# Performance work log

Hardware: AMD Instinct MI355X
Metric: run time of the kernel (lower is better)

Reference implementation:

```python
import jax, jax.numpy as jnp
import numpy as np
from jax import lax

DILATIONS = [1, 2, 4]
L, H, D_IN = 3, 256, 256
T, B = 512, 128


def _lstm_scan(gx, whh, bhh, h0, c0):
    """gx: (Td, N, 4H) precomputed input gates; scan torch LSTMCell recurrence."""
    def step(carry, g_x):
        h, c = carry
        gates = g_x + h @ whh.T + bhh          # (N, 4H), gate order i,f,g,o
        i, f, g, o = jnp.split(gates, 4, axis=-1)
        c = jax.nn.sigmoid(f) * c + jax.nn.sigmoid(i) * jnp.tanh(g)
        h = jax.nn.sigmoid(o) * jnp.tanh(c)
        return (h, c), h
    (_, _), hs = lax.scan(step, (h0, c0), gx)
    return hs                                   # (Td, N, H)


def _dilated_layer(x, wih, whh, b_ih, b_hh, rate):
    """x: (T, B, D). Pack `rate` consecutive steps along batch, run cell, unpack."""
    t, b, d = x.shape
    td = -(-t // rate)                          # ceil division
    pad = td * rate - t
    if pad:
        x = jnp.pad(x, ((0, pad), (0, 0), (0, 0)))
    h = wih.shape[0] // 4
    # torch.cat([x[i*r+j] for j in range(r)], dim=0) == reshape (td, r*b, d)
    xd = x.reshape(td, rate * b, d)
    gx = xd @ wih.T + b_ih                      # hoist input projection out of scan
    h0 = jnp.zeros((rate * b, h), x.dtype)
    hs = _lstm_scan(gx, whh, b_hh, h0, jnp.zeros_like(h0))
    # torch.chunk(out, r, 0) unroll == reshape back to (td*r, b, h), trim pad
    return hs.reshape(td * rate, b, h)[:t]


def setup_inputs() -> dict:
    key = jax.random.key(0)
    ks = jax.random.split(key, 5)
    s = 1.0 / np.sqrt(H)                        # torch LSTMCell init scale
    return {
        "x":   jax.random.normal(ks[0], (T, B, D_IN), jnp.float32),
        "Wih": jax.random.uniform(ks[1], (L, 4 * H, D_IN), jnp.float32, -s, s),
        "Whh": jax.random.uniform(ks[2], (L, 4 * H, H), jnp.float32, -s, s),
        "bih": jax.random.uniform(ks[3], (L, 4 * H), jnp.float32, -s, s),
        "bhh": jax.random.uniform(ks[4], (L, 4 * H), jnp.float32, -s, s),
    }


def reference(x, Wih, Whh, bih, bhh):
    outs = []
    cur = x
    for l, rate in enumerate(DILATIONS):
        cur = _dilated_layer(cur, Wih[l], Whh[l], bih[l], bhh[l], rate)
        outs.append(cur)
    return jnp.stack(outs, axis=0)              # (L, T, B, H)
```

## Files before the change

kernel.cpp:

```cpp
#include <hip/hip_runtime.h>


typedef _Float16 half8   __attribute__((ext_vector_type(8)));
typedef _Float16 half4_t __attribute__((ext_vector_type(4)));
typedef float    floatx4 __attribute__((ext_vector_type(4)));

__device__ __forceinline__ float sigmf(float x) {
    return 1.0f / (1.0f + __expf(-x));
}
__device__ __forceinline__ float tanhfast(float x) {
    float e = __expf(-2.0f * fabsf(x));
    float r = (1.0f - e) / (1.0f + e);
    return copysignf(r, x);
}

#define MFMA16(A, B, C) __builtin_amdgcn_mfma_f32_16x16x32_f16((A), (B), (C), 0, 0, 0)

typedef __attribute__((address_space(3))) unsigned int lds_u32;
typedef __attribute__((address_space(1))) unsigned int glb_u32;

__device__ __forceinline__ void gload_lds16(const _Float16* g, _Float16* l) {
    __builtin_amdgcn_global_load_lds((const glb_u32*)g, (lds_u32*)l, 16, 0, 0);
}

#define RING_SLOTS 4
#define RING_STRIDE (512 * 256)
#define RING_BYTES  (RING_SLOTS * RING_STRIDE * 2)
#define CNT_PER_LAYER 8192
#define CNT_INTS      24576

__global__ void prep_kernel(
    const float* __restrict__ Wih, const float* __restrict__ Whh,
    const float* __restrict__ bih, const float* __restrict__ bhh,
    _Float16* __restrict__ wihp, _Float16* __restrict__ whhp,
    float* __restrict__ biasc)
{
    int id = blockIdx.x * 256 + threadIdx.x;
    if (id < 196608) {
        int u = id;
        const float* W = Whh; _Float16* P = whhp;
        if (u >= 98304) { W = Wih; P = wihp; u -= 98304; }
        int ln = u & 63; u >>= 6;
        int ks = u & 7;  u >>= 3;
        int ct = u & 7;  u >>= 3;
        int w  = u & 7;  u >>= 3;
        int l  = u;
        int col = (ct >> 1) * 256 + w * 32 + (ct & 1) * 16 + (ln & 15);
        int k0  = ks * 32 + (ln >> 4) * 8;
        const float* src = W + ((size_t)l * 1024 + col) * 256 + k0;
        half8 hv;
#pragma unroll
        for (int j = 0; j < 8; ++j) hv[j] = (_Float16)src[j];
        *(half8*)(P + (size_t)l * 262144 +
                  (size_t)(((w * 8 + ct) * 8 + ks) * 64 + ln) * 8) = hv;
    } else if (id < 199680) {
        int v = id - 196608;
        biasc[v] = bih[v] + bhh[v];
    }
}

template<int F16IN>
__global__ __attribute__((amdgpu_flat_work_group_size(512, 512)))
__attribute__((amdgpu_waves_per_eu(2, 2)))
void gx_kernel(
    const float* __restrict__ in32,
    const _Float16* __restrict__ in16,
    const _Float16* __restrict__ wpack,
    const float* __restrict__ biasc,
    _Float16* __restrict__ gx,
    int rate, int SG, int S)
{
    __shared__ _Float16 Ab[64][264];
    const int tid = threadIdx.x, lane = tid & 63, w = tid >> 6;
    const int t = blockIdx.x / SG, sg = blockIdx.x % SG;
    const int r15 = lane & 15, q = lane >> 4;

#pragma unroll
    for (int i = 0; i < 4; ++i) {
        int id = tid + 512 * i;
        int row = id >> 5, c16 = id & 31;
        int n = sg * 64 + row;
        size_t base = ((size_t)(t * rate + (n >> 7)) * 128 + (n & 127)) * 256 + c16 * 8;
        if (F16IN) {
            *(uint4*)&Ab[row][c16 * 8] = *(const uint4*)(in16 + base);
        } else {
            floatx4 v0 = *(const floatx4*)(in32 + base);
            floatx4 v1 = *(const floatx4*)(in32 + base + 4);
            half8 hv;
            hv[0] = (_Float16)v0[0]; hv[1] = (_Float16)v0[1];
            hv[2] = (_Float16)v0[2]; hv[3] = (_Float16)v0[3];
            hv[4] = (_Float16)v1[0]; hv[5] = (_Float16)v1[1];
            hv[6] = (_Float16)v1[2]; hv[7] = (_Float16)v1[3];
            *(half8*)&Ab[row][c16 * 8] = hv;
        }
    }
    __syncthreads();

    floatx4 zero4 = {0.f, 0.f, 0.f, 0.f};
    floatx4 acc[4][8];
#pragma unroll
    for (int rt = 0; rt < 4; ++rt)
#pragma unroll
        for (int ct = 0; ct < 8; ++ct) acc[rt][ct] = zero4;

    const _Float16* wsp = wpack + (size_t)w * 32768 + (size_t)lane * 8;
    half8 bfA[8], bfB[8];
#pragma unroll
    for (int ct = 0; ct < 8; ++ct)
        bfA[ct] = *(const half8*)(wsp + (ct * 8 + 0) * 512);

#define AKS(ks, bufC, bufN) { \
    if ((ks) + 1 < 8) { _Pragma("unroll") \
        for (int ct = 0; ct < 8; ++ct) \
            bufN[ct] = *(const half8*)(wsp + (ct * 8 + ((ks) + 1)) * 512); } \
    half8 a0 = *(const half8*)&Ab[ 0 + r15][(ks) * 32 + q * 8]; \
    half8 a1 = *(const half8*)&Ab[16 + r15][(ks) * 32 + q * 8]; \
    half8 a2 = *(const half8*)&Ab[32 + r15][(ks) * 32 + q * 8]; \
    half8 a3 = *(const half8*)&Ab[48 + r15][(ks) * 32 + q * 8]; \
    _Pragma("unroll") for (int ct = 0; ct < 8; ++ct) { \
        acc[0][ct] = MFMA16(a0, bufC[ct], acc[0][ct]); \
        acc[1][ct] = MFMA16(a1, bufC[ct], acc[1][ct]); \
        acc[2][ct] = MFMA16(a2, bufC[ct], acc[2][ct]); \
        acc[3][ct] = MFMA16(a3, bufC[ct], acc[3][ct]); } }

    AKS(0, bfA, bfB); AKS(1, bfB, bfA); AKS(2, bfA, bfB); AKS(3, bfB, bfA);
    AKS(4, bfA, bfB); AKS(5, bfB, bfA); AKS(6, bfA, bfB); AKS(7, bfB, bfA);
#undef AKS

    float be[4], bo_[4];
#pragma unroll
    for (int cp = 0; cp < 4; ++cp) {
        be[cp]  = biasc[cp * 256 + w * 32 + r15];
        bo_[cp] = biasc[cp * 256 + w * 32 + 16 + r15];
    }
#pragma unroll
    for (int rt = 0; rt < 4; ++rt) {
        int sb = sg * 4 + rt;
#pragma unroll
        for (int cp = 0; cp < 4; ++cp) {
            half8 hv;
#pragma unroll
            for (int rg = 0; rg < 4; ++rg) {
                hv[rg]     = (_Float16)(acc[rt][2 * cp][rg]     + be[cp]);
                hv[4 + rg] = (_Float16)(acc[rt][2 * cp + 1][rg] + bo_[cp]);
            }
            *(half8*)(gx + ((((size_t)t * S + sb) * 8 + w) * 4 + cp) * 512 +
                      (size_t)lane * 8) = hv;
        }
    }
}

__global__ __attribute__((amdgpu_flat_work_group_size(512, 512)))
__attribute__((amdgpu_waves_per_eu(2, 2)))
void scan2_kernel(
    const _Float16* __restrict__ gx,
    const _Float16* __restrict__ wpack,
    float* __restrict__ out,
    _Float16* __restrict__ h16,
    _Float16* __restrict__ ring,
    int* __restrict__ cnt,
    int rate, int td, int NB8)
{
    __shared__ _Float16 own[2][16][136];
    __shared__ _Float16 Gx[4][4][64][8];

    const int tid  = threadIdx.x;
    const int lane = tid & 63;
    const int w    = tid >> 6;
    const int r15  = lane & 15;
    const int q    = lane >> 4;
    const int bg   = blockIdx.x % NB8;
    const int hh   = blockIdx.x / NB8;
    const int n0   = bg * 16;
    const int myb  = blockIdx.x;
    const int sib  = (hh ^ 1) * NB8 + bg;
    const int hidg = hh * 128 + w * 16 + r15;

    half8 wf[4][8];
    {
        const int w8 = hh * 4 + (w >> 1), b = w & 1;
#pragma unroll
        for (int g = 0; g < 4; ++g)
#pragma unroll
            for (int ks = 0; ks < 8; ++ks)
                wf[g][ks] = *(const half8*)(wpack +
                    (size_t)(((w8 * 8 + 2 * g + b) * 8 + ks) * 64 + lane) * 8);
    }

    for (int i = tid; i < 16 * 136; i += 512)
        (&own[0][0][0])[i] = (_Float16)0.0f;

#pragma unroll
    for (int j = 0; j < 2; ++j) {
        int gi = w * 2 + j, a = gi >> 2, part = gi & 3;
        const _Float16* src = gx +
            ((((size_t)0 * NB8 + bg) * 8 + (hh * 4 + a)) * 4 + part) * 512 +
            (size_t)lane * 8;
        gload_lds16(src, &Gx[a][part][0][0]);
    }

    float cst[4] = {0.f, 0.f, 0.f, 0.f};
    float hv[4];

    for (int t = 0; t < td; ++t) {
        const int rd = t & 1, wr = rd ^ 1;

        half8 af[8];
        if (t > 0) {
            const int ci = sib * td + (t - 1);
            if (tid == 0) {
                while (__hip_atomic_load(&cnt[ci], __ATOMIC_RELAXED,
                                         __HIP_MEMORY_SCOPE_AGENT) < 1) {
                    __builtin_amdgcn_s_sleep(1);
                }
            }
            __syncthreads();
            (void)__hip_atomic_load(&cnt[ci], __ATOMIC_ACQUIRE,
                                    __HIP_MEMORY_SCOPE_AGENT);
            const _Float16* rs = ring + (size_t)((t - 1) & 3) * RING_STRIDE +
                                 (size_t)(n0 + r15) * 256;
            if (hh == 0) {
                af[4] = *(const half8*)(rs + 4 * 32 + q * 8);
                af[5] = *(const half8*)(rs + 5 * 32 + q * 8);
                af[6] = *(const half8*)(rs + 6 * 32 + q * 8);
                af[7] = *(const half8*)(rs + 7 * 32 + q * 8);
            } else {
                af[0] = *(const half8*)(rs + 0 * 32 + q * 8);
                af[1] = *(const half8*)(rs + 1 * 32 + q * 8);
                af[2] = *(const half8*)(rs + 2 * 32 + q * 8);
                af[3] = *(const half8*)(rs + 3 * 32 + q * 8);
            }
        } else {
            __syncthreads();
            half8 z;
#pragma unroll
            for (int j = 0; j < 8; ++j) z[j] = (_Float16)0.0f;
            if (hh == 0) { af[4] = z; af[5] = z; af[6] = z; af[7] = z; }
            else         { af[0] = z; af[1] = z; af[2] = z; af[3] = z; }
        }

        floatx4 acc[4];
#pragma unroll
        for (int g = 0; g < 4; ++g) {
            half4_t gv = *(const half4_t*)&Gx[w >> 1][g][lane][(w & 1) * 4];
#pragma unroll
            for (int rg = 0; rg < 4; ++rg) acc[g][rg] = (float)gv[rg];
        }

        if (hh == 0) {
            af[0] = *(const half8*)&own[rd][r15][0 * 32 + q * 8];
            af[1] = *(const half8*)&own[rd][r15][1 * 32 + q * 8];
            af[2] = *(const half8*)&own[rd][r15][2 * 32 + q * 8];
            af[3] = *(const half8*)&own[rd][r15][3 * 32 + q * 8];
        } else {
            af[4] = *(const half8*)&own[rd][r15][0 * 32 + q * 8];
            af[5] = *(const half8*)&own[rd][r15][1 * 32 + q * 8];
            af[6] = *(const half8*)&own[rd][r15][2 * 32 + q * 8];
            af[7] = *(const half8*)&own[rd][r15][3 * 32 + q * 8];
        }

#define DO_KS(ks) { \
        acc[0] = MFMA16(af[ks], wf[0][ks], acc[0]); \
        acc[1] = MFMA16(af[ks], wf[1][ks], acc[1]); \
        acc[2] = MFMA16(af[ks], wf[2][ks], acc[2]); \
        acc[3] = MFMA16(af[ks], wf[3][ks], acc[3]); }
        if (hh == 0) {
            DO_KS(0) DO_KS(1) DO_KS(2) DO_KS(3)
            DO_KS(4) DO_KS(5) DO_KS(6) DO_KS(7)
        } else {
            DO_KS(4) DO_KS(5) DO_KS(6) DO_KS(7)
            DO_KS(0) DO_KS(1) DO_KS(2) DO_KS(3)
        }
#undef DO_KS

        _Float16* rngw = ring + (size_t)(t & 3) * RING_STRIDE;
#pragma unroll
        for (int rg = 0; rg < 4; ++rg) {
            float gi = acc[0][rg], gf = acc[1][rg];
            float gg = acc[2][rg], go = acc[3][rg];
            float c = sigmf(gf) * cst[rg] + sigmf(gi) * tanhfast(gg);
            cst[rg] = c;
            float h = sigmf(go) * tanhfast(c);
            hv[rg] = h;
            own[wr][q * 4 + rg][w * 16 + r15] = (_Float16)h;
            rngw[(size_t)(n0 + q * 4 + rg) * 256 + hidg] = (_Float16)h;
        }

        __syncthreads();
        if (tid == 0) {
            __hip_atomic_fetch_add(&cnt[myb * td + t], 1, __ATOMIC_RELEASE,
                                   __HIP_MEMORY_SCOPE_AGENT);
        }

#pragma unroll
        for (int rg = 0; rg < 4; ++rg) {
            int n = n0 + q * 4 + rg;
            int tau = t * rate + (n >> 7);
            size_t off = ((size_t)tau * 128 + (n & 127)) * 256 + hidg;
            out[off] = hv[rg];
            h16[off] = (_Float16)hv[rg];
        }

        if (t + 1 < td) {
#pragma unroll
            for (int j = 0; j < 2; ++j) {
                int gi = w * 2 + j, a = gi >> 2, part = gi & 3;
                const _Float16* src = gx +
                    ((((size_t)(t + 1) * NB8 + bg) * 8 + (hh * 4 + a)) * 4 + part) * 512 +
                    (size_t)lane * 8;
                gload_lds16(src, &Gx[a][part][0][0]);
            }
        }
    }
}

#define GH 16
#define NB 32
#define FB_CNT_INTS 6144

__global__ __launch_bounds__(256) void lstm_layer_kernel(
    const float* __restrict__ in,
    const float* __restrict__ Wih,
    const float* __restrict__ Whh,
    const float* __restrict__ bih,
    const float* __restrict__ bhh,
    float* __restrict__ out,
    _Float16* __restrict__ ring,
    int* __restrict__ cnt,
    int rate, int td, int G_b)
{
    __shared__ _Float16 Abuf[NB][520];
    __shared__ float scr[NB][68];

    const int tid  = threadIdx.x;
    const int lane = tid & 63;
    const int wv   = tid >> 6;
    const int g_b  = blockIdx.x % G_b;
    const int g_h  = blockIdx.x / G_b;
    const int hid0 = g_h * 16;
    const int n0   = g_b * NB;

    half8 bfrag[16];
    {
        const int col  = lane & 15;
        const int qq   = lane >> 4;
        const int grow = wv * 256 + hid0 + col;
        const float* wih_row = Wih + (size_t)grow * 256;
        const float* whh_row = Whh + (size_t)grow * 256;
#pragma unroll
        for (int ks = 0; ks < 16; ++ks) {
            const int k0 = ks * 32 + qq * 8;
            const float* src = (k0 < 256) ? (wih_row + k0) : (whh_row + (k0 - 256));
            floatx4 w0 = *(const floatx4*)(src);
            floatx4 w1 = *(const floatx4*)(src + 4);
            half8 hb;
            hb[0] = (_Float16)w0[0]; hb[1] = (_Float16)w0[1];
            hb[2] = (_Float16)w0[2]; hb[3] = (_Float16)w0[3];
            hb[4] = (_Float16)w1[0]; hb[5] = (_Float16)w1[1];
            hb[6] = (_Float16)w1[2]; hb[7] = (_Float16)w1[3];
            bfrag[ks] = hb;
        }
    }

    const int erow = tid >> 4;
    const int ehid = tid & 15;
    const float bi = bih[0 * 256 + hid0 + ehid] + bhh[0 * 256 + hid0 + ehid];
    const float bf = bih[1 * 256 + hid0 + ehid] + bhh[1 * 256 + hid0 + ehid];
    const float bg = bih[2 * 256 + hid0 + ehid] + bhh[2 * 256 + hid0 + ehid];
    const float bo = bih[3 * 256 + hid0 + ehid] + bhh[3 * 256 + hid0 + ehid];
    float c0 = 0.0f, c1 = 0.0f;

    floatx4 xp[8];
#pragma unroll
    for (int i = 0; i < 8; ++i) {
        int id  = tid + 256 * i;
        int row = id >> 6;
        int m   = n0 + row;
        const float* p = in + ((size_t)(0 * rate + (m >> 7)) * 128 + (m & 127)) * 256
                         + (size_t)(id & 63) * 4;
        xp[i] = *(const floatx4*)p;
    }

    for (int t = 0; t < td; ++t) {
#pragma unroll
        for (int i = 0; i < 8; ++i) {
            int id  = tid + 256 * i;
            int row = id >> 6;
            int c4  = (id & 63) * 4;
            half4_t hx;
            hx[0] = (_Float16)xp[i][0]; hx[1] = (_Float16)xp[i][1];
            hx[2] = (_Float16)xp[i][2]; hx[3] = (_Float16)xp[i][3];
            *(half4_t*)&Abuf[row][c4] = hx;
        }
        if (t + 1 < td) {
#pragma unroll
            for (int i = 0; i < 8; ++i) {
                int id  = tid + 256 * i;
                int row = id >> 6;
                int m   = n0 + row;
                const float* p = in + ((size_t)((t + 1) * rate + (m >> 7)) * 128 + (m & 127)) * 256
                                 + (size_t)(id & 63) * 4;
                xp[i] = *(const floatx4*)p;
            }
        }
        if (t > 0) {
            const int ci = g_b * td + (t - 1);
            if (tid == 0) {
                while (__hip_atomic_load(&cnt[ci], __ATOMIC_RELAXED,
                                         __HIP_MEMORY_SCOPE_AGENT) < GH) {
                    __builtin_amdgcn_s_sleep(1);
                }
            }
            __syncthreads();
            (void)__hip_atomic_load(&cnt[ci], __ATOMIC_ACQUIRE, __HIP_MEMORY_SCOPE_AGENT);
            const _Float16* rs = ring + (size_t)((t - 1) & 3) * RING_STRIDE;
#pragma unroll
            for (int i = 0; i < 4; ++i) {
                int id  = tid + 256 * i;
                int row = id >> 5;
                int kc  = id & 31;
                int m   = n0 + row;
                uint4 v = *(const uint4*)(rs + (size_t)m * 256 + kc * 8);
                *(uint4*)&Abuf[row][256 + kc * 8] = v;
            }
        } else {
#pragma unroll
            for (int i = 0; i < 4; ++i) {
                int id  = tid + 256 * i;
                int row = id >> 5;
                int kc  = id & 31;
                uint4 z = {0u, 0u, 0u, 0u};
                *(uint4*)&Abuf[row][256 + kc * 8] = z;
            }
        }
        __syncthreads();

        floatx4 acc0 = {0.f, 0.f, 0.f, 0.f};
        floatx4 acc1 = {0.f, 0.f, 0.f, 0.f};
        {
            const int r  = lane & 15;
            const int qq = lane >> 4;
#pragma unroll
            for (int ks = 0; ks < 16; ++ks) {
                half8 a0 = *(const half8*)&Abuf[r][ks * 32 + qq * 8];
                half8 a1 = *(const half8*)&Abuf[16 + r][ks * 32 + qq * 8];
                acc0 = MFMA16(a0, bfrag[ks], acc0);
                acc1 = MFMA16(a1, bfrag[ks], acc1);
            }
        }
        {
            const int r  = lane & 15;
            const int qq = lane >> 4;
#pragma unroll
            for (int reg = 0; reg < 4; ++reg) {
                scr[qq * 4 + reg][wv * 16 + r]      = acc0[reg];
                scr[16 + qq * 4 + reg][wv * 16 + r] = acc1[reg];
            }
        }
        __syncthreads();

        {
            float gi0 = scr[erow][ehid]           + bi;
            float gf0 = scr[erow][16 + ehid]      + bf;
            float gg0 = scr[erow][32 + ehid]      + bg;
            float go0 = scr[erow][48 + ehid]      + bo;
            float gi1 = scr[16 + erow][ehid]      + bi;
            float gf1 = scr[16 + erow][16 + ehid] + bf;
            float gg1 = scr[16 + erow][32 + ehid] + bg;
            float go1 = scr[16 + erow][48 + ehid] + bo;

            c0 = sigmf(gf0) * c0 + sigmf(gi0) * tanhfast(gg0);
            c1 = sigmf(gf1) * c1 + sigmf(gi1) * tanhfast(gg1);
            float h0v = sigmf(go0) * tanhfast(c0);
            float h1v = sigmf(go1) * tanhfast(c1);

            int m0 = n0 + erow, m1 = m0 + 16;
            int tau0 = t * rate + (m0 >> 7);
            int tau1 = t * rate + (m1 >> 7);
            out[((size_t)tau0 * 128 + (m0 & 127)) * 256 + hid0 + ehid] = h0v;
            out[((size_t)tau1 * 128 + (m1 & 127)) * 256 + hid0 + ehid] = h1v;

            _Float16* rw_ = ring + (size_t)(t & 3) * RING_STRIDE;
            rw_[(size_t)m0 * 256 + hid0 + ehid] = (_Float16)h0v;
            rw_[(size_t)m1 * 256 + hid0 + ehid] = (_Float16)h1v;
        }

        __syncthreads();
        if (tid == 0) {
            __hip_atomic_fetch_add(&cnt[g_b * td + t], 1, __ATOMIC_RELEASE,
                                   __HIP_MEMORY_SCOPE_AGENT);
        }
    }
}

extern "C" void kernel_launch(void* const* d_in, const int* in_sizes, int n_in,
                              void* d_out, int out_size, void* d_ws, size_t ws_size,
                              hipStream_t stream) {
    const float* x   = (const float*)d_in[0];
    const float* Wih = (const float*)d_in[1];
    const float* Whh = (const float*)d_in[2];
    const float* bih = (const float*)d_in[3];
    const float* bhh = (const float*)d_in[4];
    float* out = (float*)d_out;

    const size_t GX_BYTES   = 134217728ull;
    const size_t H16_BYTES  = 33554432ull;
    const size_t WP_BYTES   = 1572864ull;
    const size_t BIAS_BYTES = 12288ull;
    const size_t NEED = GX_BYTES + H16_BYTES + 2 * WP_BYTES + BIAS_BYTES +
                        RING_BYTES + CNT_INTS * sizeof(int);

    if (ws_size >= NEED) {
        char* p = (char*)d_ws;
        _Float16* gxb  = (_Float16*)p;                 p += GX_BYTES;
        _Float16* h16  = (_Float16*)p;                 p += H16_BYTES;
        _Float16* whhp = (_Float16*)p;                 p += WP_BYTES;
        _Float16* wihp = (_Float16*)p;                 p += WP_BYTES;
        float*    biasc= (float*)p;                    p += BIAS_BYTES;
        _Float16* ring = (_Float16*)p;                 p += RING_BYTES;
        int*      cnt  = (int*)p;

        hipMemsetAsync(cnt, 0, CNT_INTS * sizeof(int), stream);
        prep_kernel<<<dim3(780), dim3(256), 0, stream>>>(
            Wih, Whh, bih, bhh, wihp, whhp, biasc);

        const int rates[3] = {1, 2, 4};
        for (int l = 0; l < 3; ++l) {
            const int rate = rates[l];
            const int td   = 512 / rate;
            const int NB8  = rate * 8;
            const int SG   = NB8 / 4;
            float* out_l = out + (size_t)l * 512 * 128 * 256;
            if (l == 0)
                gx_kernel<0><<<dim3(td * SG), dim3(512), 0, stream>>>(
                    x, nullptr, wihp + (size_t)l * 262144, biasc + l * 1024,
                    gxb, rate, SG, NB8);
            else
                gx_kernel<1><<<dim3(td * SG), dim3(512), 0, stream>>>(
                    nullptr, h16, wihp + (size_t)l * 262144, biasc + l * 1024,
                    gxb, rate, SG, NB8);
            scan2_kernel<<<dim3(2 * NB8), dim3(512), 0, stream>>>(
                gxb, whhp + (size_t)l * 262144, out_l, h16, ring,
                cnt + l * CNT_PER_LAYER, rate, td, NB8);
        }
        return;
    }

    _Float16* ring = (_Float16*)d_ws;
    int* cnt = (int*)((char*)d_ws + RING_BYTES);
    hipMemsetAsync(cnt, 0, FB_CNT_INTS * sizeof(int), stream);

    const int rates[3]  = {1, 2, 4};
    const int cntOff[3] = {0, 2048, 4096};
    const float* in_ptr = x;
    for (int l = 0; l < 3; ++l) {
        const int rate = rates[l];
        const int td   = 512 / rate;
        const int N    = rate * 128;
        const int G_b  = N / NB;
        lstm_layer_kernel<<<dim3(G_b * GH), dim3(256), 0, stream>>>(
            in_ptr,
            Wih + (size_t)l * 1024 * 256,
            Whh + (size_t)l * 1024 * 256,
            bih + (size_t)l * 1024,
            bhh + (size_t)l * 1024,
            out + (size_t)l * 512 * 128 * 256,
            ring, cnt + cntOff[l],
            rate, td, G_b);
        in_ptr = out + (size_t)l * 512 * 128 * 256;
    }
}
```

Measured before the change: 5.221 ms.

## Split LSTM scan across four hidden-quarter blocks with swizzled LDS h exchange

The recurrent scan now splits each batch group's hidden dimension across four 256-thread blocks instead of two 512-thread blocks. Each block waits on its three peers per step, then stages the full previous h from a two-slot global ring into XOR-swizzled LDS via direct global-to-LDS loads. Gate activations are regrouped through an fp32 LDS scratch so each thread does vectorized elementwise math and vector stores. The input-projection kernel is retiled into four times as many blocks, each computing a narrower column slice. The intent is more CUs working on the latency-bound recurrence, at the cost of more cross-block synchronization, extra barriers and global-memory traffic for the h exchange.

```diff
diff --git a/kernel.cpp b/kernel.cpp
--- a/kernel.cpp
+++ b/kernel.cpp
@@ -23,11 +23,11 @@
     __builtin_amdgcn_global_load_lds((const glb_u32*)g, (lds_u32*)l, 16, 0, 0);
 }
 
-#define RING_SLOTS 4
 #define RING_STRIDE (512 * 256)
-#define RING_BYTES  (RING_SLOTS * RING_STRIDE * 2)
-#define CNT_PER_LAYER 8192
-#define CNT_INTS      24576
+#define BR_SLOTS    2
+#define BR_RING_BYTES (BR_SLOTS * RING_STRIDE * 2)
+#define CNT_PER_LAYER 16384
+#define CNT_INTS      49152
 
 __global__ void prep_kernel(
     const float* __restrict__ Wih, const float* __restrict__ Whh,
@@ -60,26 +60,28 @@
 }
 
 template<int F16IN>
-__global__ __attribute__((amdgpu_flat_work_group_size(512, 512)))
-__attribute__((amdgpu_waves_per_eu(2, 2)))
-void gx_kernel(
+__global__ __launch_bounds__(512, 1) void gx_kernel(
     const float* __restrict__ in32,
     const _Float16* __restrict__ in16,
     const _Float16* __restrict__ wpack,
     const float* __restrict__ biasc,
     _Float16* __restrict__ gx,
-    int rate, int SG, int S)
+    int rate, int RB, int NB8)
 {
     __shared__ _Float16 Ab[64][264];
     const int tid = threadIdx.x, lane = tid & 63, w = tid >> 6;
-    const int t = blockIdx.x / SG, sg = blockIdx.x % SG;
+    const int cb  = blockIdx.x & 3;
+    const int nbi = (blockIdx.x >> 2) % RB;
+    const int t   = (blockIdx.x >> 2) / RB;
     const int r15 = lane & 15, q = lane >> 4;
+    const int w8  = 2 * cb + (w & 1);
+    const int cp  = w >> 1;
 
 #pragma unroll
     for (int i = 0; i < 4; ++i) {
         int id = tid + 512 * i;
         int row = id >> 5, c16 = id & 31;
-        int n = sg * 64 + row;
+        int n = nbi * 64 + row;
         size_t base = ((size_t)(t * rate + (n >> 7)) * 128 + (n & 127)) * 256 + c16 * 8;
         if (F16IN) {
             *(uint4*)&Ab[row][c16 * 8] = *(const uint4*)(in16 + base);
@@ -97,62 +99,43 @@
     __syncthreads();
 
     floatx4 zero4 = {0.f, 0.f, 0.f, 0.f};
-    floatx4 acc[4][8];
-#pragma unroll
-    for (int rt = 0; rt < 4; ++rt)
-#pragma unroll
-        for (int ct = 0; ct < 8; ++ct) acc[rt][ct] = zero4;
-
-    const _Float16* wsp = wpack + (size_t)w * 32768 + (size_t)lane * 8;
-    half8 bfA[8], bfB[8];
-#pragma unroll
-    for (int ct = 0; ct < 8; ++ct)
-        bfA[ct] = *(const half8*)(wsp + (ct * 8 + 0) * 512);
-
-#define AKS(ks, bufC, bufN) { \
-    if ((ks) + 1 < 8) { _Pragma("unroll") \
-        for (int ct = 0; ct < 8; ++ct) \
-            bufN[ct] = *(const half8*)(wsp + (ct * 8 + ((ks) + 1)) * 512); } \
-    half8 a0 = *(const half8*)&Ab[ 0 + r15][(ks) * 32 + q * 8]; \
-    half8 a1 = *(const half8*)&Ab[16 + r15][(ks) * 32 + q * 8]; \
-    half8 a2 = *(const half8*)&Ab[32 + r15][(ks) * 32 + q * 8]; \
-    half8 a3 = *(const half8*)&Ab[48 + r15][(ks) * 32 + q * 8]; \
-    _Pragma("unroll") for (int ct = 0; ct < 8; ++ct) { \
-        acc[0][ct] = MFMA16(a0, bufC[ct], acc[0][ct]); \
-        acc[1][ct] = MFMA16(a1, bufC[ct], acc[1][ct]); \
-        acc[2][ct] = MFMA16(a2, bufC[ct], acc[2][ct]); \
-        acc[3][ct] = MFMA16(a3, bufC[ct], acc[3][ct]); } }
-
-    AKS(0, bfA, bfB); AKS(1, bfB, bfA); AKS(2, bfA, bfB); AKS(3, bfB, bfA);
-    AKS(4, bfA, bfB); AKS(5, bfB, bfA); AKS(6, bfA, bfB); AKS(7, bfB, bfA);
-#undef AKS
-
-    float be[4], bo_[4];
-#pragma unroll
-    for (int cp = 0; cp < 4; ++cp) {
-        be[cp]  = biasc[cp * 256 + w * 32 + r15];
-        bo_[cp] = biasc[cp * 256 + w * 32 + 16 + r15];
-    }
+    floatx4 acc[4][2];
+#pragma unroll
+    for (int rt = 0; rt < 4; ++rt) { acc[rt][0] = zero4; acc[rt][1] = zero4; }
+
+    const _Float16* wb = wpack + (size_t)((w8 * 8 + 2 * cp) * 8) * 512 +
+                         (size_t)lane * 8;
+#pragma unroll
+    for (int ks = 0; ks < 8; ++ks) {
+        half8 bf0 = *(const half8*)(wb + (size_t)(0 * 8 + ks) * 512);
+        half8 bf1 = *(const half8*)(wb + (size_t)(1 * 8 + ks) * 512);
+        half8 a0 = *(const half8*)&Ab[ 0 + r15][ks * 32 + q * 8];
+        half8 a1 = *(const half8*)&Ab[16 + r15][ks * 32 + q * 8];
+        half8 a2 = *(const half8*)&Ab[32 + r15][ks * 32 + q * 8];
+        half8 a3 = *(const half8*)&Ab[48 + r15][ks * 32 + q * 8];
+        acc[0][0] = MFMA16(a0, bf0, acc[0][0]); acc[0][1] = MFMA16(a0, bf1, acc[0][1]);
+        acc[1][0] = MFMA16(a1, bf0, acc[1][0]); acc[1][1] = MFMA16(a1, bf1, acc[1][1]);
+        acc[2][0] = MFMA16(a2, bf0, acc[2][0]); acc[2][1] = MFMA16(a2, bf1, acc[2][1]);
+        acc[3][0] = MFMA16(a3, bf0, acc[3][0]); acc[3][1] = MFMA16(a3, bf1, acc[3][1]);
+    }
+
+    const float be0 = biasc[cp * 256 + w8 * 32 + r15];
+    const float be1 = biasc[cp * 256 + w8 * 32 + 16 + r15];
 #pragma unroll
     for (int rt = 0; rt < 4; ++rt) {
-        int sb = sg * 4 + rt;
-#pragma unroll
-        for (int cp = 0; cp < 4; ++cp) {
-            half8 hv;
-#pragma unroll
-            for (int rg = 0; rg < 4; ++rg) {
-                hv[rg]     = (_Float16)(acc[rt][2 * cp][rg]     + be[cp]);
-                hv[4 + rg] = (_Float16)(acc[rt][2 * cp + 1][rg] + bo_[cp]);
-            }
-            *(half8*)(gx + ((((size_t)t * S + sb) * 8 + w) * 4 + cp) * 512 +
-                      (size_t)lane * 8) = hv;
-        }
-    }
-}
-
-__global__ __attribute__((amdgpu_flat_work_group_size(512, 512)))
-__attribute__((amdgpu_waves_per_eu(2, 2)))
-void scan2_kernel(
+        int bg = nbi * 4 + rt;
+        half8 hv;
+#pragma unroll
+        for (int rg = 0; rg < 4; ++rg) {
+            hv[rg]     = (_Float16)(acc[rt][0][rg] + be0);
+            hv[4 + rg] = (_Float16)(acc[rt][1][rg] + be1);
+        }
+        *(half8*)(gx + ((((size_t)t * NB8 + bg) * 8 + w8) * 4 + cp) * 512 +
+                  (size_t)lane * 8) = hv;
+    }
+}
+
+__global__ __launch_bounds__(256, 1) void scan4_kernel(
     const _Float16* __restrict__ gx,
     const _Float16* __restrict__ wpack,
     float* __restrict__ out,
@@ -161,161 +144,145 @@
     int* __restrict__ cnt,
     int rate, int td, int NB8)
 {
-    __shared__ _Float16 own[2][16][136];
-    __shared__ _Float16 Gx[4][4][64][8];
+    __shared__ _Float16 Hs[4096];
+    __shared__ float scr[16][260];
 
     const int tid  = threadIdx.x;
     const int lane = tid & 63;
-    const int w    = tid >> 6;
+    const int wv   = tid >> 6;
     const int r15  = lane & 15;
     const int q    = lane >> 4;
     const int bg   = blockIdx.x % NB8;
-    const int hh   = blockIdx.x / NB8;
+    const int hb   = blockIdx.x / NB8;
     const int n0   = bg * 16;
     const int myb  = blockIdx.x;
-    const int sib  = (hh ^ 1) * NB8 + bg;
-    const int hidg = hh * 128 + w * 16 + r15;
-
+
+    const _Float16* wsl = wpack + (size_t)(2 * hb) * 64 * 512;
     half8 wf[4][8];
-    {
-        const int w8 = hh * 4 + (w >> 1), b = w & 1;
-#pragma unroll
-        for (int g = 0; g < 4; ++g)
-#pragma unroll
-            for (int ks = 0; ks < 8; ++ks)
-                wf[g][ks] = *(const half8*)(wpack +
-                    (size_t)(((w8 * 8 + 2 * g + b) * 8 + ks) * 64 + lane) * 8);
-    }
-
-    for (int i = tid; i < 16 * 136; i += 512)
-        (&own[0][0][0])[i] = (_Float16)0.0f;
-
-#pragma unroll
-    for (int j = 0; j < 2; ++j) {
-        int gi = w * 2 + j, a = gi >> 2, part = gi & 3;
-        const _Float16* src = gx +
-            ((((size_t)0 * NB8 + bg) * 8 + (hh * 4 + a)) * 4 + part) * 512 +
-            (size_t)lane * 8;
-        gload_lds16(src, &Gx[a][part][0][0]);
+#pragma unroll
+    for (int ht = 0; ht < 4; ++ht) {
+        const int ct8 = 2 * wv + (ht & 1);
+        const int w8r = ht >> 1;
+#pragma unroll
+        for (int ks = 0; ks < 8; ++ks) {
+            wf[ht][ks] = *(const half8*)(wsl +
+                (size_t)(((w8r * 8 + ct8) * 8 + ks) * 64 + lane) * 8);
+            asm volatile("" : "+v"(wf[ht][ks]));
+        }
     }
 
     float cst[4] = {0.f, 0.f, 0.f, 0.f};
-    float hv[4];
+
+    half8 gxc[2];
+#pragma unroll
+    for (int w8r = 0; w8r < 2; ++w8r)
+        gxc[w8r] = *(const half8*)(gx +
+            ((((size_t)0 * NB8 + bg) * 8 + (2 * hb + w8r)) * 4 + wv) * 512 +
+            (size_t)lane * 8);
 
     for (int t = 0; t < td; ++t) {
-        const int rd = t & 1, wr = rd ^ 1;
-
-        half8 af[8];
         if (t > 0) {
-            const int ci = sib * td + (t - 1);
-            if (tid == 0) {
+            if ((tid & 63) == 0 && wv < 3) {
+                int s = wv + (wv >= hb ? 1 : 0);
+                const int ci = (s * NB8 + bg) * td + (t - 1);
                 while (__hip_atomic_load(&cnt[ci], __ATOMIC_RELAXED,
-                                         __HIP_MEMORY_SCOPE_AGENT) < 1) {
+                                         __HIP_MEMORY_SCOPE_AGENT) < 1)
                     __builtin_amdgcn_s_sleep(1);
-                }
             }
             __syncthreads();
-            (void)__hip_atomic_load(&cnt[ci], __ATOMIC_ACQUIRE,
+            (void)__hip_atomic_load(&cnt[myb * td + (t - 1)], __ATOMIC_ACQUIRE,
                                     __HIP_MEMORY_SCOPE_AGENT);
-            const _Float16* rs = ring + (size_t)((t - 1) & 3) * RING_STRIDE +
-                                 (size_t)(n0 + r15) * 256;
-            if (hh == 0) {
-                af[4] = *(const half8*)(rs + 4 * 32 + q * 8);
-                af[5] = *(const half8*)(rs + 5 * 32 + q * 8);
-                af[6] = *(const half8*)(rs + 6 * 32 + q * 8);
-                af[7] = *(const half8*)(rs + 7 * 32 + q * 8);
-            } else {
-                af[0] = *(const half8*)(rs + 0 * 32 + q * 8);
-                af[1] = *(const half8*)(rs + 1 * 32 + q * 8);
-                af[2] = *(const half8*)(rs + 2 * 32 + q * 8);
-                af[3] = *(const half8*)(rs + 3 * 32 + q * 8);
+            const _Float16* rs = ring + (size_t)((t - 1) & 1) * RING_STRIDE +
+                                 (size_t)n0 * 256;
+#pragma unroll
+            for (int jj = 0; jj < 2; ++jj) {
+                int c = wv * 2 + jj;
+                int D = c * 1024 + lane * 16;
+                int row = D >> 9;
+                int O = D ^ ((row & 7) << 4);
+                gload_lds16(rs + (O >> 1), Hs + c * 512);
             }
         } else {
             __syncthreads();
-            half8 z;
-#pragma unroll
-            for (int j = 0; j < 8; ++j) z[j] = (_Float16)0.0f;
-            if (hh == 0) { af[4] = z; af[5] = z; af[6] = z; af[7] = z; }
-            else         { af[0] = z; af[1] = z; af[2] = z; af[3] = z; }
-        }
-
+            uint4 z = {0u, 0u, 0u, 0u};
+            *(uint4*)((char*)Hs + tid * 32)      = z;
+            *(uint4*)((char*)Hs + tid * 32 + 16) = z;
+        }
+        __syncthreads();
+
+        half8 af[8];
+#pragma unroll
+        for (int ks = 0; ks < 8; ++ks) {
+            const int bo = r15 * 512 + ((ks * 64 + q * 16) ^ ((r15 & 7) << 4));
+            af[ks] = *(const half8*)((const char*)Hs + bo);
+        }
         floatx4 acc[4];
 #pragma unroll
-        for (int g = 0; g < 4; ++g) {
-            half4_t gv = *(const half4_t*)&Gx[w >> 1][g][lane][(w & 1) * 4];
-#pragma unroll
-            for (int rg = 0; rg < 4; ++rg) acc[g][rg] = (float)gv[rg];
-        }
-
-        if (hh == 0) {
-            af[0] = *(const half8*)&own[rd][r15][0 * 32 + q * 8];
-            af[1] = *(const half8*)&own[rd][r15][1 * 32 + q * 8];
-            af[2] = *(const half8*)&own[rd][r15][2 * 32 + q * 8];
-            af[3] = *(const half8*)&own[rd][r15][3 * 32 + q * 8];
-        } else {
-            af[4] = *(const half8*)&own[rd][r15][0 * 32 + q * 8];
-            af[5] = *(const half8*)&own[rd][r15][1 * 32 + q * 8];
-            af[6] = *(const half8*)&own[rd][r15][2 * 32 + q * 8];
-            af[7] = *(const half8*)&own[rd][r15][3 * 32 + q * 8];
-        }
-
-#define DO_KS(ks) { \
-        acc[0] = MFMA16(af[ks], wf[0][ks], acc[0]); \
-        acc[1] = MFMA16(af[ks], wf[1][ks], acc[1]); \
-        acc[2] = MFMA16(af[ks], wf[2][ks], acc[2]); \
-        acc[3] = MFMA16(af[ks], wf[3][ks], acc[3]); }
-        if (hh == 0) {
-            DO_KS(0) DO_KS(1) DO_KS(2) DO_KS(3)
-            DO_KS(4) DO_KS(5) DO_KS(6) DO_KS(7)
-        } else {
-            DO_KS(4) DO_KS(5) DO_KS(6) DO_KS(7)
-            DO_KS(0) DO_KS(1) DO_KS(2) DO_KS(3)
-        }
-#undef DO_KS
-
-        _Float16* rngw = ring + (size_t)(t & 3) * RING_STRIDE;
-#pragma unroll
-        for (int rg = 0; rg < 4; ++rg) {
-            float gi = acc[0][rg], gf = acc[1][rg];
-            float gg = acc[2][rg], go = acc[3][rg];
-            float c = sigmf(gf) * cst[rg] + sigmf(gi) * tanhfast(gg);
-            cst[rg] = c;
-            float h = sigmf(go) * tanhfast(c);
-            hv[rg] = h;
-            own[wr][q * 4 + rg][w * 16 + r15] = (_Float16)h;
-            rngw[(size_t)(n0 + q * 4 + rg) * 256 + hidg] = (_Float16)h;
-        }
-
+        for (int ht = 0; ht < 4; ++ht)
+#pragma unroll
+            for (int rg = 0; rg < 4; ++rg)
+                acc[ht][rg] = (float)gxc[ht >> 1][(ht & 1) * 4 + rg];
+
+#pragma unroll
+        for (int ks = 0; ks < 8; ++ks) {
+            acc[0] = MFMA16(af[ks], wf[0][ks], acc[0]);
+            acc[1] = MFMA16(af[ks], wf[1][ks], acc[1]);
+            acc[2] = MFMA16(af[ks], wf[2][ks], acc[2]);
+            acc[3] = MFMA16(af[ks], wf[3][ks], acc[3]);
+        }
+
+#pragma unroll
+        for (int ht = 0; ht < 4; ++ht)
+#pragma unroll
+            for (int rg = 0; rg < 4; ++rg)
+                scr[q * 4 + rg][wv * 64 + ht * 16 + r15] = acc[ht][rg];
         __syncthreads();
-        if (tid == 0) {
+
+        {
+            const int row  = tid >> 4;
+            const int hid4 = (tid & 15) * 4;
+            floatx4 gi = *(const floatx4*)&scr[row][  0 + hid4];
+            floatx4 gf = *(const floatx4*)&scr[row][ 64 + hid4];
+            floatx4 gg = *(const floatx4*)&scr[row][128 + hid4];
+            floatx4 go = *(const floatx4*)&scr[row][192 + hid4];
+            floatx4 ov; half4_t hh;
+#pragma unroll
+            for (int c2 = 0; c2 < 4; ++c2) {
+                float cc = sigmf(gf[c2]) * cst[c2] + sigmf(gi[c2]) * tanhfast(gg[c2]);
+                cst[c2] = cc;
+                float h = sigmf(go[c2]) * tanhfast(cc);
+                ov[c2] = h; hh[c2] = (_Float16)h;
+            }
+            const int n    = n0 + row;
+            const int tau  = t * rate + (n >> 7);
+            const int hidg = hb * 64 + hid4;
+            size_t off = ((size_t)tau * 128 + (n & 127)) * 256 + hidg;
+            *(floatx4*)(out + off) = ov;
+            *(half4_t*)(h16 + off) = hh;
+            _Float16* rw_ = ring + (size_t)(t & 1) * RING_STRIDE;
+            *(half4_t*)(rw_ + (size_t)n * 256 + hidg) = hh;
+        }
+
+        __syncthreads();
+        if (tid == 0)
             __hip_atomic_fetch_add(&cnt[myb * td + t], 1, __ATOMIC_RELEASE,
                                    __HIP_MEMORY_SCOPE_AGENT);
-        }
-
-#pragma unroll
-        for (int rg = 0; rg < 4; ++rg) {
-            int n = n0 + q * 4 + rg;
-            int tau = t * rate + (n >> 7);
-            size_t off = ((size_t)tau * 128 + (n & 127)) * 256 + hidg;
-            out[off] = hv[rg];
-            h16[off] = (_Float16)hv[rg];
-        }
-
-        if (t + 1 < td) {
-#pragma unroll
-            for (int j = 0; j < 2; ++j) {
-                int gi = w * 2 + j, a = gi >> 2, part = gi & 3;
-                const _Float16* src = gx +
-                    ((((size_t)(t + 1) * NB8 + bg) * 8 + (hh * 4 + a)) * 4 + part) * 512 +
-                    (size_t)lane * 8;
-                gload_lds16(src, &Gx[a][part][0][0]);
-            }
+
+        {
+            const int tn = (t + 1 < td) ? (t + 1) : t;
+#pragma unroll
+            for (int w8r = 0; w8r < 2; ++w8r)
+                gxc[w8r] = *(const half8*)(gx +
+                    ((((size_t)tn * NB8 + bg) * 8 + (2 * hb + w8r)) * 4 + wv) * 512 +
+                    (size_t)lane * 8);
         }
     }
 }
 
 #define GH 16
 #define NB 32
+#define FB_RING_SLOTS 4
+#define FB_RING_BYTES (FB_RING_SLOTS * RING_STRIDE * 2)
 #define FB_CNT_INTS 6144
 
 __global__ __launch_bounds__(256) void lstm_layer_kernel(
@@ -508,19 +475,19 @@
     const size_t WP_BYTES   = 1572864ull;
     const size_t BIAS_BYTES = 12288ull;
     const size_t NEED = GX_BYTES + H16_BYTES + 2 * WP_BYTES + BIAS_BYTES +
-                        RING_BYTES + CNT_INTS * sizeof(int);
+                        BR_RING_BYTES + (size_t)CNT_INTS * 4;
 
     if (ws_size >= NEED) {
         char* p = (char*)d_ws;
-        _Float16* gxb  = (_Float16*)p;                 p += GX_BYTES;
-        _Float16* h16  = (_Float16*)p;                 p += H16_BYTES;
-        _Float16* whhp = (_Float16*)p;                 p += WP_BYTES;
-        _Float16* wihp = (_Float16*)p;                 p += WP_BYTES;
-        float*    biasc= (float*)p;                    p += BIAS_BYTES;
-        _Float16* ring = (_Float16*)p;                 p += RING_BYTES;
-        int*      cnt  = (int*)p;
-
-        hipMemsetAsync(cnt, 0, CNT_INTS * sizeof(int), stream);
+        _Float16* gxb   = (_Float16*)p;                p += GX_BYTES;
+        _Float16* h16   = (_Float16*)p;                p += H16_BYTES;
+        _Float16* whhp  = (_Float16*)p;                p += WP_BYTES;
+        _Float16* wihp  = (_Float16*)p;                p += WP_BYTES;
+        float*    biasc = (float*)p;                   p += BIAS_BYTES;
+        _Float16* ring  = (_Float16*)p;                p += BR_RING_BYTES;
+        int*      cnt   = (int*)p;
+
+        hipMemsetAsync(cnt, 0, (size_t)CNT_INTS * 4, stream);
         prep_kernel<<<dim3(780), dim3(256), 0, stream>>>(
             Wih, Whh, bih, bhh, wihp, whhp, biasc);
 
@@ -529,17 +496,17 @@
             const int rate = rates[l];
             const int td   = 512 / rate;
             const int NB8  = rate * 8;
-            const int SG   = NB8 / 4;
+            const int RB   = rate * 2;
             float* out_l = out + (size_t)l * 512 * 128 * 256;
             if (l == 0)
-                gx_kernel<0><<<dim3(td * SG), dim3(512), 0, stream>>>(
+                gx_kernel<0><<<dim3(td * RB * 4), dim3(512), 0, stream>>>(
                     x, nullptr, wihp + (size_t)l * 262144, biasc + l * 1024,
-                    gxb, rate, SG, NB8);
+                    gxb, rate, RB, NB8);
             else
-                gx_kernel<1><<<dim3(td * SG), dim3(512), 0, stream>>>(
+                gx_kernel<1><<<dim3(td * RB * 4), dim3(512), 0, stream>>>(
                     nullptr, h16, wihp + (size_t)l * 262144, biasc + l * 1024,
-                    gxb, rate, SG, NB8);
-            scan2_kernel<<<dim3(2 * NB8), dim3(512), 0, stream>>>(
+                    gxb, rate, RB, NB8);
+            scan4_kernel<<<dim3(4 * NB8), dim3(256), 0, stream>>>(
                 gxb, whhp + (size_t)l * 262144, out_l, h16, ring,
                 cnt + l * CNT_PER_LAYER, rate, td, NB8);
         }
@@ -547,7 +514,7 @@
     }
 
     _Float16* ring = (_Float16*)d_ws;
-    int* cnt = (int*)((char*)d_ws + RING_BYTES);
+    int* cnt = (int*)((char*)d_ws + FB_RING_BYTES);
     hipMemsetAsync(cnt, 0, FB_CNT_INTS * sizeof(int), stream);
 
     const int rates[3]  = {1, 2, 4};
```

Measured after the change: 4.615 ms. 11.6% less time.
